# Optimization experiments

Hardware: AMD Instinct MI355X
Metric: run time of the kernel (lower is better)

## Reference

```python
import jax, jax.numpy as jnp
import numpy as np

N = 100000   # nodes
E = 640000   # directed edges
H = 128      # hidden_channels
C = 7        # dataset_num_classes
G = 64       # graphs in the batch
F_IN = 1     # dataset_num_node_features


def setup_inputs() -> dict:
    key = jax.random.key(0)
    ks = jax.random.split(key, 12)
    x = jax.random.normal(ks[0], (N, F_IN), jnp.float32)
    edge_index = jax.random.randint(ks[1], (2, E), 0, N, dtype=jnp.int32)
    batch = jnp.sort(jax.random.randint(ks[2], (N,), 0, G, dtype=jnp.int32))

    def glorot(k, fan_in, fan_out):
        s = jnp.sqrt(6.0 / (fan_in + fan_out)).astype(jnp.float32)
        return jax.random.uniform(k, (fan_in, fan_out), jnp.float32, -s, s)

    return {
        "x": x, "edge_index": edge_index, "batch": batch,
        "W1": glorot(ks[3], F_IN, H), "b1": jnp.zeros((H,), jnp.float32),
        "W2": glorot(ks[4], H, H),    "b2": jnp.zeros((H,), jnp.float32),
        "W3": glorot(ks[5], H, H),    "b3": jnp.zeros((H,), jnp.float32),
        "Wl": glorot(ks[6], H, C),    "bl": jnp.zeros((C,), jnp.float32),
    }


def reference(x, edge_index, batch, W1, b1, W2, b2, W3, b3, Wl, bl):
    n = x.shape[0]
    loop = jnp.arange(n, dtype=edge_index.dtype)
    row = jnp.concatenate([edge_index[0], loop])  # source (message origin)
    col = jnp.concatenate([edge_index[1], loop])  # target (aggregation dst)
    # symmetric normalization D^-1/2 (A+I) D^-1/2 (PyG GCNConv default)
    deg = jax.ops.segment_sum(jnp.ones(row.shape[0], x.dtype), col, num_segments=n)
    dinv = jax.lax.rsqrt(jnp.maximum(deg, 1.0))  # deg >= 1 due to self-loops
    norm = dinv[row] * dinv[col]                 # [E+N]

    def gcn_conv(h, W, b):
        h = h @ W                                # transform first (PyG order)
        msg = h[row] * norm[:, None]             # gather + scale, [E+N, H]
        return jax.ops.segment_sum(msg, col, num_segments=n) + b

    h = jax.nn.relu(gcn_conv(x, W1, b1))
    h = jax.nn.relu(gcn_conv(h, W2, b2))
    h = gcn_conv(h, W3, b3)

    # global mean pool over graph ids; dropout is identity in eval mode
    counts = jax.ops.segment_sum(jnp.ones(n, h.dtype), batch, num_segments=G)
    pooled = jax.ops.segment_sum(h, batch, num_segments=G) / jnp.maximum(counts, 1.0)[:, None]
    return pooled @ Wl + bl
```

## Files before the change

kernel.cpp:

```cpp
#include <hip/hip_runtime.h>

#define HDIM 128
#define NGRAPH 64
#define NCLASS 7
#define PG_NODES 128
#define MAXB 2048

typedef __attribute__((ext_vector_type(8))) __bf16 bf16x8;
typedef __attribute__((ext_vector_type(4))) float f32x4;

__device__ __forceinline__ unsigned short bf16_rne(float f) {
  unsigned u = __float_as_uint(f);
  u += 0x7FFF + ((u >> 16) & 1);
  return (unsigned short)(u >> 16);
}

__device__ __forceinline__ void gload16(const void* g, void* l) {
  __builtin_amdgcn_global_load_lds((const __attribute__((address_space(1))) void*)g,
                                   (__attribute__((address_space(3))) void*)l, 16, 0, 0);
}


__global__ void k_countw(const int* __restrict__ col, const int* __restrict__ row, int E,
                         int* __restrict__ histI, int* __restrict__ histO,
                         const float* __restrict__ W,
                         unsigned short* __restrict__ wthi, unsigned short* __restrict__ wtlo,
                         int cB, int NB) {
  int b = blockIdx.x;
  if (b < cB) {
    __shared__ int binsI[MAXB], binsO[MAXB];
    int t = threadIdx.x;
    for (int i = t; i < NB; i += 256) { binsI[i] = 0; binsO[i] = 0; }
    __syncthreads();
    int base = b << 11;
#pragma unroll
    for (int j = 0; j < 8; j++) {
      int e = base + (j << 8) + t;
      if (e < E) {
        atomicAdd(&binsI[col[e] >> 6], 1);
        atomicAdd(&binsO[row[e] >> 6], 1);
      }
    }
    __syncthreads();
    for (int i = t; i < NB; i += 256) {
      histI[(size_t)b * NB + i] = binsI[i];
      histO[(size_t)b * NB + i] = binsO[i];
    }
  } else {
    int idx = (b - cB) * 256 + threadIdx.x;
    int c = idx >> 7, k = idx & 127;
    float v = W[k * 128 + c];
    unsigned short h = bf16_rne(v);
    wthi[idx] = h;
    wtlo[idx] = bf16_rne(v - __uint_as_float((unsigned)h << 16));
  }
}

__global__ void k_hA(int* __restrict__ histI, int* __restrict__ histO,
                     int* __restrict__ segI, int* __restrict__ segO,
                     int NB, int cB) {
  int bkt = blockIdx.x * 256 + threadIdx.x;
  if (bkt >= NB) return;
  int* hist = blockIdx.z ? histO : histI;
  int* segs = blockIdx.z ? segO : segI;
  int r0 = blockIdx.y << 3;
  int v[8];
#pragma unroll
  for (int j = 0; j < 8; j++) {
    int ri = r0 + j;
    v[j] = (ri < cB) ? hist[(size_t)ri * NB + bkt] : 0;
  }
  int s = 0;
#pragma unroll
  for (int j = 0; j < 8; j++) { int tv = v[j]; v[j] = s; s += tv; }
#pragma unroll
  for (int j = 0; j < 8; j++) {
    int ri = r0 + j;
    if (ri < cB) hist[(size_t)ri * NB + bkt] = v[j];
  }
  segs[(size_t)blockIdx.y * NB + bkt] = s;
}

__global__ void k_hB(int* __restrict__ segI, int* __restrict__ segO,
                     int* __restrict__ btotI, int* __restrict__ btotO,
                     int NB, int NSEG) {
  int bkt = blockIdx.x * 256 + threadIdx.x;
  if (bkt >= NB) return;
  int* segs = blockIdx.y ? segO : segI;
  int* btot = blockIdx.y ? btotO : btotI;
  int run = 0;
  for (int c0 = 0; c0 < NSEG; c0 += 8) {
    int v[8];
#pragma unroll
    for (int j = 0; j < 8; j++) {
      int si = c0 + j;
      v[j] = (si < NSEG) ? segs[(size_t)si * NB + bkt] : 0;
    }
#pragma unroll
    for (int j = 0; j < 8; j++) { int tv = v[j]; v[j] = run; run += tv; }
#pragma unroll
    for (int j = 0; j < 8; j++) {
      int si = c0 + j;
      if (si < NSEG) segs[(size_t)si * NB + bkt] = v[j];
    }
  }
  btot[bkt] = run;
}

__global__ void k_hscanB(const int* __restrict__ btotI, int* __restrict__ boffI,
                         const int* __restrict__ btotO, int* __restrict__ boffO,
                         int NB, int E) {
  __shared__ int sh[1024];
  int t = threadIdx.x;
  for (int s = 0; s < 2; s++) {
    const int* src = s ? btotO : btotI;
    int* boff = s ? boffO : boffI;
    int i0 = 2 * t, i1 = 2 * t + 1;
    int a0 = (i0 < NB) ? src[i0] : 0;
    int a1 = (i1 < NB) ? src[i1] : 0;
    sh[t] = a0 + a1;
    __syncthreads();
    for (int o = 1; o < 1024; o <<= 1) {
      int v = (t >= o) ? sh[t - o] : 0;
      __syncthreads();
      sh[t] += v;
      __syncthreads();
    }
    int ex = (t == 0) ? 0 : sh[t - 1];
    if (i0 < NB) boff[i0] = ex;
    if (i1 < NB) boff[i1] = ex + a0;
    if (t == 0) boff[NB] = E;
    __syncthreads();
  }
}

__global__ void __launch_bounds__(256) k_fill(const int* __restrict__ row,
                                              const int* __restrict__ col, int E,
                                              const int* __restrict__ histI,
                                              const int* __restrict__ histO,
                                              const int* __restrict__ segI,
                                              const int* __restrict__ segO,
                                              const int* __restrict__ boffI,
                                              const int* __restrict__ boffO,
                                              int* __restrict__ inBL,
                                              int* __restrict__ outBL, int NB) {
  __shared__ int baseI[MAXB], baseO[MAXB], binsI[MAXB], binsO[MAXB];
  int t = threadIdx.x, b = blockIdx.x;
  int sg = b >> 3;
  for (int i = t; i < NB; i += 256) {
    baseI[i] = boffI[i] + segI[(size_t)sg * NB + i] + histI[(size_t)b * NB + i];
    baseO[i] = boffO[i] + segO[(size_t)sg * NB + i] + histO[(size_t)b * NB + i];
    binsI[i] = 0;
    binsO[i] = 0;
  }
  __syncthreads();
  int base = b << 11;
#pragma unroll
  for (int j = 0; j < 8; j++) {
    int e = base + (j << 8) + t;
    if (e < E) {
      int r = row[e], c = col[e];
      int rkI = atomicAdd(&binsI[c >> 6], 1);
      int rkO = atomicAdd(&binsO[r >> 6], 1);
      inBL[baseI[c >> 6] + rkI] = (r << 6) | (c & 63);
      outBL[baseO[r >> 6] + rkO] = (c << 6) | (r & 63);
    }
  }
}

__global__ void __launch_bounds__(256) k_rank2x(const int* __restrict__ inBL,
                                                const int* __restrict__ boffI,
                                                const int* __restrict__ batch,
                                                const float* __restrict__ x,
                                                int2* __restrict__ od,
                                                float2* __restrict__ dx,
                                                int* __restrict__ gwi, int n) {
  __shared__ int cnt[64], cnt2[64], loc[64], sc[64];
  int bi = blockIdx.x, t = threadIdx.x;
  if (t < 64) { cnt[t] = 0; cnt2[t] = 0; }
  __syncthreads();
  int e0 = boffI[bi], e1 = boffI[bi + 1];
  for (int e = e0 + t; e < e1; e += 256) atomicAdd(&cnt[inBL[e] & 63], 1);
  __syncthreads();
  if (t < 64) sc[t] = cnt[t];
  __syncthreads();
  for (int o = 1; o < 64; o <<= 1) {
    int v = (t < 64 && t >= o) ? sc[t - o] : 0;
    __syncthreads();
    if (t < 64) sc[t] += v;
    __syncthreads();
  }
  if (t < 64) {
    int excl = (t == 0) ? 0 : sc[t - 1];
    loc[t] = e0 + excl;
    int node = (bi << 6) + t;
    if (node < n) {
      int g = batch[node];
      float dinv = rsqrtf((float)(cnt[t] + 1));
      od[node] = make_int2((e0 + excl) | (g << 24), __float_as_int(dinv));
      dx[node] = make_float2(dinv, x[node]);
    }
  }
  __syncthreads();
  for (int e = e0 + t; e < e1; e += 256) {
    int v = inBL[e];
    int dl = v & 63;
    int k = atomicAdd(&cnt2[dl], 1);
    gwi[loc[dl] + k] = v >> 6;
  }
}

__global__ void k_s(const int2* __restrict__ od, const float2* __restrict__ dx,
                    const int* __restrict__ gwi, float2* __restrict__ sd, int n, int E) {
  int i = blockIdx.x * 256 + threadIdx.x;
  if (i >= n) return;
  int2 o2 = od[i];
  float dinv = __int_as_float(o2.y);
  int e0 = o2.x & 0xFFFFFF;
  int e1 = (i + 1 < n) ? (od[i + 1].x & 0xFFFFFF) : E;
  float s0 = 0.f, s1 = 0.f;
  int e = e0;
  for (; e + 2 <= e1; e += 2) {
    float2 a = dx[gwi[e]];
    float2 b = dx[gwi[e + 1]];
    s0 = fmaf(a.x, a.y, s0);
    s1 = fmaf(b.x, b.y, s1);
  }
  if (e < e1) { float2 a = dx[gwi[e]]; s0 = fmaf(a.x, a.y, s0); }
  float xv = dx[i].y;
  sd[i] = make_float2(fmaf(dinv * dinv, xv, dinv * (s0 + s1)), dinv);
}


__global__ void __launch_bounds__(256) k_l2in(const float2* __restrict__ sd,
                                              const int2* __restrict__ od,
                                              const int* __restrict__ gwi,
                                              const float* __restrict__ W1,
                                              const float* __restrict__ b1,
                                              ushort2* __restrict__ zhi,
                                              ushort2* __restrict__ zlo, int n, int E) {
  int node = blockIdx.x * 4 + (threadIdx.x >> 6);
  if (node >= n) return;
  int l = threadIdx.x & 63;
  float2 w1 = ((const float2*)W1)[l];
  float2 bv = ((const float2*)b1)[l];
  int2 on = od[node];
  float dstd = __int_as_float(on.y);
  float nself = dstd * dstd;
  float sv = sd[node].x;
  float2 acc;
  acc.x = nself * fmaxf(fmaf(sv, w1.x, bv.x), 0.f);
  acc.y = nself * fmaxf(fmaf(sv, w1.y, bv.y), 0.f);
  int e0 = on.x & 0xFFFFFF;
  int e1 = (node + 1 < n) ? (od[node + 1].x & 0xFFFFFF) : E;

  for (int eb = e0; eb < e1; eb += 64) {
    int m = e1 - eb; if (m > 64) m = 64;
    int ee = eb + l; if (ee >= e1) ee = e1 - 1;
    float2 q = sd[gwi[ee]];
    float u = q.y * dstd;
    int k = 0;
    for (; k + 4 <= m; k += 4) {
      float q0 = __shfl(q.x, k),     u0 = __shfl(u, k);
      float q1 = __shfl(q.x, k + 1), u1 = __shfl(u, k + 1);
      float q2 = __shfl(q.x, k + 2), u2 = __shfl(u, k + 2);
      float q3 = __shfl(q.x, k + 3), u3 = __shfl(u, k + 3);
      acc.x = fmaf(u0, fmaxf(fmaf(q0, w1.x, bv.x), 0.f), acc.x);
      acc.y = fmaf(u0, fmaxf(fmaf(q0, w1.y, bv.y), 0.f), acc.y);
      acc.x = fmaf(u1, fmaxf(fmaf(q1, w1.x, bv.x), 0.f), acc.x);
      acc.y = fmaf(u1, fmaxf(fmaf(q1, w1.y, bv.y), 0.f), acc.y);
      acc.x = fmaf(u2, fmaxf(fmaf(q2, w1.x, bv.x), 0.f), acc.x);
      acc.y = fmaf(u2, fmaxf(fmaf(q2, w1.y, bv.y), 0.f), acc.y);
      acc.x = fmaf(u3, fmaxf(fmaf(q3, w1.x, bv.x), 0.f), acc.x);
      acc.y = fmaf(u3, fmaxf(fmaf(q3, w1.y, bv.y), 0.f), acc.y);
    }
    for (; k < m; k++) {
      float qk = __shfl(q.x, k), uk = __shfl(u, k);
      acc.x = fmaf(uk, fmaxf(fmaf(qk, w1.x, bv.x), 0.f), acc.x);
      acc.y = fmaf(uk, fmaxf(fmaf(qk, w1.y, bv.y), 0.f), acc.y);
    }
  }

  ushort2 h, lo;
  h.x = bf16_rne(acc.x);
  lo.x = bf16_rne(acc.x - __uint_as_float((unsigned)h.x << 16));
  h.y = bf16_rne(acc.y);
  lo.y = bf16_rne(acc.y - __uint_as_float((unsigned)h.y << 16));
  zhi[(size_t)node * 64 + l] = h;
  zlo[(size_t)node * 64 + l] = lo;
}


__global__ void __launch_bounds__(256)
k_gemm_mfma(const unsigned short* __restrict__ zhi, const unsigned short* __restrict__ zlo,
            const unsigned short* __restrict__ whi, const unsigned short* __restrict__ wlo,
            const float* __restrict__ bias, float* __restrict__ out, int n) {
  __shared__ uint4 lds[2048];
  const int t = threadIdx.x;
  const int l = t & 63, wv = t >> 6;
  const int wr = wv >> 1, wc = wv & 1;
  const int lr = l & 15, lk = l >> 4;
  const int rowBase = blockIdx.x << 7;
  const bool full = (rowBase + 128 <= n);

  f32x4 acc[4][4];
#pragma unroll
  for (int mt = 0; mt < 4; mt++)
#pragma unroll
    for (int nt = 0; nt < 4; nt++) acc[mt][nt] = (f32x4){0.f, 0.f, 0.f, 0.f};

  for (int ch = 0; ch < 4; ch++) {
    __syncthreads();
    if (full) {
#pragma unroll
      for (int i = 0; i < 2; i++) {
        int s = t + (i << 8);
        int sl = s & 63, rt = s >> 6;
        int row = rowBase + (rt << 4) + (sl & 15);
        int kk = (ch << 5) + ((sl >> 4) << 3);
        gload16(&zhi[(size_t)row * 128 + kk], &lds[s]);
        gload16(&zlo[(size_t)row * 128 + kk], &lds[512 + s]);
      }
    } else {
#pragma unroll
      for (int i = 0; i < 2; i++) {
        int s = t + (i << 8);
        int sl = s & 63, rt = s >> 6;
        int row = rowBase + (rt << 4) + (sl & 15);
        int kk = (ch << 5) + ((sl >> 4) << 3);
        uint4 vh = make_uint4(0u, 0u, 0u, 0u), vl = vh;
        if (row < n) {
          vh = *(const uint4*)&zhi[(size_t)row * 128 + kk];
          vl = *(const uint4*)&zlo[(size_t)row * 128 + kk];
        }
        lds[s] = vh;
        lds[512 + s] = vl;
      }
    }
#pragma unroll
    for (int i = 0; i < 2; i++) {
      int s = t + (i << 8);
      int sl = s & 63, ct = s >> 6;
      int col = (ct << 4) + (sl & 15);
      int kk = (ch << 5) + ((sl >> 4) << 3);
      gload16(&whi[col * 128 + kk], &lds[1024 + s]);
      gload16(&wlo[col * 128 + kk], &lds[1536 + s]);
    }
    __syncthreads();

    bf16x8 ah[4], al[4], bh[4], bl[4];
#pragma unroll
    for (int mt = 0; mt < 4; mt++) {
      int slot = ((wr << 2) + mt) * 64 + l;
      ah[mt] = *(const bf16x8*)&lds[slot];
      al[mt] = *(const bf16x8*)&lds[512 + slot];
    }
#pragma unroll
    for (int nt = 0; nt < 4; nt++) {
      int slot = ((wc << 2) + nt) * 64 + l;
      bh[nt] = *(const bf16x8*)&lds[1024 + slot];
      bl[nt] = *(const bf16x8*)&lds[1536 + slot];
    }
#pragma unroll
    for (int mt = 0; mt < 4; mt++)
#pragma unroll
      for (int nt = 0; nt < 4; nt++) {
        acc[mt][nt] = __builtin_amdgcn_mfma_f32_16x16x32_bf16(ah[mt], bh[nt], acc[mt][nt], 0, 0, 0);
        acc[mt][nt] = __builtin_amdgcn_mfma_f32_16x16x32_bf16(ah[mt], bl[nt], acc[mt][nt], 0, 0, 0);
        acc[mt][nt] = __builtin_amdgcn_mfma_f32_16x16x32_bf16(al[mt], bh[nt], acc[mt][nt], 0, 0, 0);
      }
  }

  float bv[4];
#pragma unroll
  for (int nt = 0; nt < 4; nt++) bv[nt] = bias[(wc << 6) + (nt << 4) + lr];
#pragma unroll
  for (int mt = 0; mt < 4; mt++) {
    int rbase = rowBase + (wr << 6) + (mt << 4) + (lk << 2);
#pragma unroll
    for (int j = 0; j < 4; j++) {
      int row = rbase + j;
      if (row < n) {
#pragma unroll
        for (int nt = 0; nt < 4; nt++) {
          int c2 = (wc << 6) + (nt << 4) + lr;
          out[(size_t)row * 128 + c2] = fmaxf(acc[mt][nt][j] + bv[nt], 0.f);
        }
      }
    }
  }
}


__global__ void __launch_bounds__(256) k_pgemm(const float* __restrict__ H,
                                               const int* __restrict__ outBL,
                                               const int* __restrict__ boff,
                                               const int2* __restrict__ od,
                                               float* __restrict__ partials, int n) {
  __shared__ float4 Hl4[64 * 32];
  __shared__ float4 Pl4[64 * 16];
  __shared__ float dinvL[64];
  float* Pl = (float*)Pl4;
  const int t = threadIdx.x;
  const int jl = t & 31;
  const int gq = (t >> 5) << 1;
  float4 acc[8];
#pragma unroll
  for (int i = 0; i < 8; i++) acc[i] = make_float4(0.f, 0.f, 0.f, 0.f);
  const int base0 = blockIdx.x * PG_NODES;

  for (int sub = 0; sub < PG_NODES / 64; sub++) {
    const int base = base0 + sub * 64;
    __syncthreads();
    if (base + 64 <= n) {
      for (int l = t; l < 2048; l += 256)
        gload16(&H[(size_t)(base + (l >> 5)) * 128 + ((l & 31) << 2)], &Hl4[l]);
    } else {
      for (int l = t; l < 2048; l += 256) {
        int i = l >> 5, q = l & 31;
        int node = base + i;
        Hl4[l] = (node < n) ? *(const float4*)&H[(size_t)node * 128 + (q << 2)]
                            : make_float4(0.f, 0.f, 0.f, 0.f);
      }
    }
    for (int l = t; l < 1024; l += 256) Pl4[l] = make_float4(0.f, 0.f, 0.f, 0.f);
    __syncthreads();
    if (t < 64) {
      int node = base + t;
      float dv = 0.f;
      if (node < n) {
        int2 o2 = od[node];
        dv = __int_as_float(o2.y);
        atomicAdd(&Pl[(t << 6) + (int)(((unsigned)o2.x) >> 24)], dv * dv);
      }
      dinvL[t] = dv;
    }
    __syncthreads();
    int e0 = 0, e1 = 0;
    if (base < n) {
      int bi = base >> 6;
      e0 = boff[bi];
      e1 = boff[bi + 1];
    }
    for (int e = e0 + t; e < e1; e += 256) {
      int p = outBL[e];
      int2 oc = od[p >> 6];
      float w2 = dinvL[p & 63] * __int_as_float(oc.y);
      atomicAdd(&Pl[((p & 63) << 6) + (int)(((unsigned)oc.x) >> 24)], w2);
    }
    __syncthreads();

#define FMA4(A, PV) \
  A.x = fmaf(PV, hv.x, A.x); A.y = fmaf(PV, hv.y, A.y); \
  A.z = fmaf(PV, hv.z, A.z); A.w = fmaf(PV, hv.w, A.w);
#pragma unroll 4
    for (int i = 0; i < 64; i++) {
      float4 hv = Hl4[i * 32 + jl];
      float4 pa = Pl4[i * 16 + gq];
      float4 pb = Pl4[i * 16 + gq + 1];
      FMA4(acc[0], pa.x) FMA4(acc[1], pa.y) FMA4(acc[2], pa.z) FMA4(acc[3], pa.w)
      FMA4(acc[4], pb.x) FMA4(acc[5], pb.y) FMA4(acc[6], pb.z) FMA4(acc[7], pb.w)
    }
#undef FMA4
  }

  float* dst = &partials[(size_t)blockIdx.x * (NGRAPH * HDIM)];
  int gb = (t >> 5) << 3;
#pragma unroll
  for (int gi = 0; gi < 8; gi++)
    *(float4*)&dst[(gb + gi) * HDIM + (jl << 2)] = acc[gi];
}

__global__ void k_reduce(const float* __restrict__ partials, float* __restrict__ pooled,
                         int nparts) {
  int cell = blockIdx.x * 256 + threadIdx.x;
  int stride = gridDim.y;
  int p = blockIdx.y;
  float a0 = 0.f, a1 = 0.f, a2 = 0.f, a3 = 0.f;
  for (; p + 3 * stride < nparts; p += 4 * stride) {
    a0 += partials[(size_t)p * 8192 + cell];
    a1 += partials[(size_t)(p + stride) * 8192 + cell];
    a2 += partials[(size_t)(p + 2 * stride) * 8192 + cell];
    a3 += partials[(size_t)(p + 3 * stride) * 8192 + cell];
  }
  for (; p < nparts; p += stride) a0 += partials[(size_t)p * 8192 + cell];
  unsafeAtomicAdd(&pooled[cell], (a0 + a1) + (a2 + a3));
}

__global__ void k_mid(const float* __restrict__ pooled, const int* __restrict__ batch, int n,
                      const float* __restrict__ W3, const float* __restrict__ b3,
                      const float* __restrict__ Wl, const float* __restrict__ bl,
                      float* __restrict__ out) {
  __shared__ float sh[HDIM];
  __shared__ float invSh;
  int g = blockIdx.x, j = threadIdx.x;
  if (j == 0) {
    int lo = 0, hi = n;
    while (lo < hi) { int m = (lo + hi) >> 1; if (batch[m] < g) lo = m + 1; else hi = m; }
    int a = lo;
    lo = 0; hi = n;
    while (lo < hi) { int m = (lo + hi) >> 1; if (batch[m] < g + 1) lo = m + 1; else hi = m; }
    invSh = 1.f / fmaxf((float)(lo - a), 1.f);
  }
  __syncthreads();
  float inv = invSh;
  float acc = 0.f;
  for (int k = 0; k < HDIM; k++) acc = fmaf(pooled[g * HDIM + k], W3[k * HDIM + j], acc);
  sh[j] = acc * inv + b3[j];
  __syncthreads();
  if (j < NCLASS) {
    float o = bl[j];
    for (int k = 0; k < HDIM; k++) o = fmaf(sh[k], Wl[k * NCLASS + j], o);
    out[g * NCLASS + j] = o;
  }
}


extern "C" void kernel_launch(void* const* d_in, const int* in_sizes, int n_in,
                              void* d_out, int out_size, void* d_ws, size_t ws_size,
                              hipStream_t stream) {
  const float* x   = (const float*)d_in[0];
  const int*   ei  = (const int*)d_in[1];
  const int*   bat = (const int*)d_in[2];
  const float* W1  = (const float*)d_in[3];
  const float* b1  = (const float*)d_in[4];
  const float* W2  = (const float*)d_in[5];
  const float* b2  = (const float*)d_in[6];
  const float* W3  = (const float*)d_in[7];
  const float* b3  = (const float*)d_in[8];
  const float* Wl  = (const float*)d_in[9];
  const float* bl  = (const float*)d_in[10];
  float* out = (float*)d_out;

  const int n = in_sizes[0];
  const int E = in_sizes[1] / 2;
  const int* rowv = ei;
  const int* colv = ei + E;
  const int NB = (n + 63) >> 6;
  const int cB = (E + 2047) / 2048;
  const int NSEG = (cB + 7) >> 3;

  char* w = (char*)d_ws;
  size_t o = 0;
  auto alloc = [&](size_t bytes) {
    size_t r = (o + 255) & ~(size_t)255;
    o = r + bytes;
    return r;
  };
  const int nPB = (n + PG_NODES - 1) / PG_NODES;

  size_t o_pool  = alloc((size_t)NGRAPH * HDIM * 4);
  size_t zero_end = o;
  size_t o_histI = alloc((size_t)cB * NB * 4);
  size_t o_histO = alloc((size_t)cB * NB * 4);
  size_t o_segI  = alloc((size_t)NSEG * NB * 4);
  size_t o_segO  = alloc((size_t)NSEG * NB * 4);
  size_t o_btotI = alloc((size_t)MAXB * 4);
  size_t o_btotO = alloc((size_t)MAXB * 4);
  size_t o_boffI = alloc((size_t)(MAXB + 1) * 4);
  size_t o_boffO = alloc((size_t)(MAXB + 1) * 4);
  size_t o_od    = alloc((size_t)n * 8);
  size_t o_dx    = alloc((size_t)n * 8);
  size_t o_sd    = alloc((size_t)n * 8);
  size_t o_wt    = alloc((size_t)HDIM * HDIM * 4);
  size_t o_gw    = alloc((size_t)E * 4);
  size_t o_inBL  = alloc((size_t)E * 4);
  size_t o_outBL = alloc((size_t)E * 4);
  size_t o_bufA  = alloc((size_t)n * HDIM * 4);
  size_t o_bufB  = alloc((size_t)n * HDIM * 4);
  (void)n_in; (void)out_size; (void)ws_size;

  float*  pooled   = (float*)(w + o_pool);
  int*    histI    = (int*)(w + o_histI);
  int*    histO    = (int*)(w + o_histO);
  int*    segI     = (int*)(w + o_segI);
  int*    segO     = (int*)(w + o_segO);
  int*    btotI    = (int*)(w + o_btotI);
  int*    btotO    = (int*)(w + o_btotO);
  int*    boffI    = (int*)(w + o_boffI);
  int*    boffO    = (int*)(w + o_boffO);
  int2*   od       = (int2*)(w + o_od);
  float2* dx       = (float2*)(w + o_dx);
  float2* sd       = (float2*)(w + o_sd);
  unsigned short* wthi = (unsigned short*)(w + o_wt);
  unsigned short* wtlo = wthi + HDIM * HDIM;
  int*    gwi      = (int*)(w + o_gw);
  int*    inBL     = (int*)(w + o_inBL);
  int*    outBL    = (int*)(w + o_outBL);
  float*  bufA     = (float*)(w + o_bufA);
  unsigned short* zhi = (unsigned short*)(w + o_bufB);
  unsigned short* zlo = zhi + (size_t)n * HDIM;
  float*  partials = (float*)(w + o_bufB);

  hipMemsetAsync(w + o_pool, 0, zero_end - o_pool, stream);

  const int gB = (NB + 255) / 256;
  k_countw<<<cB + 64, 256, 0, stream>>>(colv, rowv, E, histI, histO, W2,
                                        wthi, wtlo, cB, NB);
  k_hA<<<dim3(gB, NSEG, 2), 256, 0, stream>>>(histI, histO, segI, segO, NB, cB);
  k_hB<<<dim3(gB, 2), 256, 0, stream>>>(segI, segO, btotI, btotO, NB, NSEG);
  k_hscanB<<<1, 1024, 0, stream>>>(btotI, boffI, btotO, boffO, NB, E);
  k_fill<<<cB, 256, 0, stream>>>(rowv, colv, E, histI, histO, segI, segO,
                                 boffI, boffO, inBL, outBL, NB);
  k_rank2x<<<NB, 256, 0, stream>>>(inBL, boffI, bat, x, od, dx, gwi, n);
  k_s<<<(n + 255) / 256, 256, 0, stream>>>(od, dx, gwi, sd, n, E);

  k_l2in<<<(n + 3) / 4, 256, 0, stream>>>(sd, od, gwi, W1, b1,
                                          (ushort2*)zhi, (ushort2*)zlo, n, E);

  k_gemm_mfma<<<(n + 127) / 128, 256, 0, stream>>>(zhi, zlo, wthi, wtlo, b2, bufA, n);

  k_pgemm<<<nPB, 256, 0, stream>>>(bufA, outBL, boffO, od, partials, n);
  k_reduce<<<dim3(32, 8), 256, 0, stream>>>(partials, pooled, nPB);

  k_mid<<<NGRAPH, HDIM, 0, stream>>>(pooled, bat, n, W3, b3, Wl, bl, out);
}
```

Before: 250.0 us.

## Fuse MFMA layer-2 GEMM with pooled-propagation GEMM via shared LDS union

Merges the bf16-split MFMA GEMM kernel and the per-block pooling GEMM into one kernel. The relu'd GEMM tile stays in registers and is written to an LDS union instead of round-tripping a full N x 128 fp32 buffer through global memory. This removes one kernel launch and about 100 MB of global write and read traffic. In exchange, LDS use per block grows to about 48 KB, which may lower occupancy, and partials now get their own workspace allocation.

Result: faster. 242.8 us (-2.8%).

```diff
diff --git a/kernel.cpp b/kernel.cpp
--- a/kernel.cpp
+++ b/kernel.cpp
@@ -3,7 +3,6 @@
 #define HDIM 128
 #define NGRAPH 64
 #define NCLASS 7
-#define PG_NODES 128
 #define MAXB 2048
 
 typedef __attribute__((ext_vector_type(8))) __bf16 bf16x8;
@@ -291,11 +290,19 @@
 }
 
 
+union SmemU {
+  uint4 stage[2048];
+  struct { float Hf[64 * 128]; float Pl[64 * 64]; } pg;
+};
+
 __global__ void __launch_bounds__(256)
-k_gemm_mfma(const unsigned short* __restrict__ zhi, const unsigned short* __restrict__ zlo,
-            const unsigned short* __restrict__ whi, const unsigned short* __restrict__ wlo,
-            const float* __restrict__ bias, float* __restrict__ out, int n) {
-  __shared__ uint4 lds[2048];
+k_gemm_pg(const unsigned short* __restrict__ zhi, const unsigned short* __restrict__ zlo,
+          const unsigned short* __restrict__ whi, const unsigned short* __restrict__ wlo,
+          const float* __restrict__ bias, const int* __restrict__ outBL,
+          const int* __restrict__ boffO, const int2* __restrict__ od,
+          float* __restrict__ partials, int n) {
+  __shared__ SmemU u;
+  __shared__ float dinvL[64];
   const int t = threadIdx.x;
   const int l = t & 63, wv = t >> 6;
   const int wr = wv >> 1, wc = wv & 1;
@@ -318,8 +325,8 @@
         int sl = s & 63, rt = s >> 6;
         int row = rowBase + (rt << 4) + (sl & 15);
         int kk = (ch << 5) + ((sl >> 4) << 3);
-        gload16(&zhi[(size_t)row * 128 + kk], &lds[s]);
-        gload16(&zlo[(size_t)row * 128 + kk], &lds[512 + s]);
+        gload16(&zhi[(size_t)row * 128 + kk], &u.stage[s]);
+        gload16(&zlo[(size_t)row * 128 + kk], &u.stage[512 + s]);
       }
     } else {
 #pragma unroll
@@ -333,8 +340,8 @@
           vh = *(const uint4*)&zhi[(size_t)row * 128 + kk];
           vl = *(const uint4*)&zlo[(size_t)row * 128 + kk];
         }
-        lds[s] = vh;
-        lds[512 + s] = vl;
+        u.stage[s] = vh;
+        u.stage[512 + s] = vl;
       }
     }
 #pragma unroll
@@ -343,8 +350,8 @@
       int sl = s & 63, ct = s >> 6;
       int col = (ct << 4) + (sl & 15);
       int kk = (ch << 5) + ((sl >> 4) << 3);
-      gload16(&whi[col * 128 + kk], &lds[1024 + s]);
-      gload16(&wlo[col * 128 + kk], &lds[1536 + s]);
+      gload16(&whi[col * 128 + kk], &u.stage[1024 + s]);
+      gload16(&wlo[col * 128 + kk], &u.stage[1536 + s]);
     }
     __syncthreads();
 
@@ -352,14 +359,14 @@
 #pragma unroll
     for (int mt = 0; mt < 4; mt++) {
       int slot = ((wr << 2) + mt) * 64 + l;
-      ah[mt] = *(const bf16x8*)&lds[slot];
-      al[mt] = *(const bf16x8*)&lds[512 + slot];
+      ah[mt] = *(const bf16x8*)&u.stage[slot];
+      al[mt] = *(const bf16x8*)&u.stage[512 + slot];
     }
 #pragma unroll
     for (int nt = 0; nt < 4; nt++) {
       int slot = ((wc << 2) + nt) * 64 + l;
-      bh[nt] = *(const bf16x8*)&lds[1024 + slot];
-      bl[nt] = *(const bf16x8*)&lds[1536 + slot];
+      bh[nt] = *(const bf16x8*)&u.stage[1024 + slot];
+      bl[nt] = *(const bf16x8*)&u.stage[1536 + slot];
     }
 #pragma unroll
     for (int mt = 0; mt < 4; mt++)
@@ -375,55 +382,35 @@
 #pragma unroll
   for (int nt = 0; nt < 4; nt++) bv[nt] = bias[(wc << 6) + (nt << 4) + lr];
 #pragma unroll
-  for (int mt = 0; mt < 4; mt++) {
-    int rbase = rowBase + (wr << 6) + (mt << 4) + (lk << 2);
-#pragma unroll
-    for (int j = 0; j < 4; j++) {
-      int row = rbase + j;
-      if (row < n) {
-#pragma unroll
-        for (int nt = 0; nt < 4; nt++) {
-          int c2 = (wc << 6) + (nt << 4) + lr;
-          out[(size_t)row * 128 + c2] = fmaxf(acc[mt][nt][j] + bv[nt], 0.f);
-        }
-      }
-    }
-  }
-}
-
-
-__global__ void __launch_bounds__(256) k_pgemm(const float* __restrict__ H,
-                                               const int* __restrict__ outBL,
-                                               const int* __restrict__ boff,
-                                               const int2* __restrict__ od,
-                                               float* __restrict__ partials, int n) {
-  __shared__ float4 Hl4[64 * 32];
-  __shared__ float4 Pl4[64 * 16];
-  __shared__ float dinvL[64];
-  float* Pl = (float*)Pl4;
-  const int t = threadIdx.x;
+  for (int mt = 0; mt < 4; mt++)
+#pragma unroll
+    for (int nt = 0; nt < 4; nt++)
+#pragma unroll
+      for (int j = 0; j < 4; j++)
+        acc[mt][nt][j] = fmaxf(acc[mt][nt][j] + bv[nt], 0.f);
+
   const int jl = t & 31;
   const int gq = (t >> 5) << 1;
-  float4 acc[8];
-#pragma unroll
-  for (int i = 0; i < 8; i++) acc[i] = make_float4(0.f, 0.f, 0.f, 0.f);
-  const int base0 = blockIdx.x * PG_NODES;
-
-  for (int sub = 0; sub < PG_NODES / 64; sub++) {
-    const int base = base0 + sub * 64;
-    __syncthreads();
-    if (base + 64 <= n) {
-      for (int l = t; l < 2048; l += 256)
-        gload16(&H[(size_t)(base + (l >> 5)) * 128 + ((l & 31) << 2)], &Hl4[l]);
-    } else {
-      for (int l = t; l < 2048; l += 256) {
-        int i = l >> 5, q = l & 31;
-        int node = base + i;
-        Hl4[l] = (node < n) ? *(const float4*)&H[(size_t)node * 128 + (q << 2)]
-                            : make_float4(0.f, 0.f, 0.f, 0.f);
-      }
-    }
-    for (int l = t; l < 1024; l += 256) Pl4[l] = make_float4(0.f, 0.f, 0.f, 0.f);
+  float4 acc2[8];
+#pragma unroll
+  for (int i = 0; i < 8; i++) acc2[i] = make_float4(0.f, 0.f, 0.f, 0.f);
+
+  for (int sub = 0; sub < 2; sub++) {
+    const int base = rowBase + (sub << 6);
+    __syncthreads();
+    for (int i4 = t; i4 < 1024; i4 += 256) ((float4*)u.pg.Pl)[i4] = make_float4(0.f, 0.f, 0.f, 0.f);
+    if (wr == sub) {
+#pragma unroll
+      for (int mt = 0; mt < 4; mt++)
+#pragma unroll
+        for (int j = 0; j < 4; j++) {
+          int li = (mt << 4) + (lk << 2) + j;
+          bool ok = (base + li) < n;
+#pragma unroll
+          for (int nt = 0; nt < 4; nt++)
+            u.pg.Hf[li * 128 + (wc << 6) + (nt << 4) + lr] = ok ? acc[mt][nt][j] : 0.f;
+        }
+    }
     __syncthreads();
     if (t < 64) {
       int node = base + t;
@@ -431,7 +418,7 @@
       if (node < n) {
         int2 o2 = od[node];
         dv = __int_as_float(o2.y);
-        atomicAdd(&Pl[(t << 6) + (int)(((unsigned)o2.x) >> 24)], dv * dv);
+        atomicAdd(&u.pg.Pl[(t << 6) + (int)(((unsigned)o2.x) >> 24)], dv * dv);
       }
       dinvL[t] = dv;
     }
@@ -439,14 +426,14 @@
     int e0 = 0, e1 = 0;
     if (base < n) {
       int bi = base >> 6;
-      e0 = boff[bi];
-      e1 = boff[bi + 1];
+      e0 = boffO[bi];
+      e1 = boffO[bi + 1];
     }
     for (int e = e0 + t; e < e1; e += 256) {
       int p = outBL[e];
       int2 oc = od[p >> 6];
       float w2 = dinvL[p & 63] * __int_as_float(oc.y);
-      atomicAdd(&Pl[((p & 63) << 6) + (int)(((unsigned)oc.x) >> 24)], w2);
+      atomicAdd(&u.pg.Pl[((p & 63) << 6) + (int)(((unsigned)oc.x) >> 24)], w2);
     }
     __syncthreads();
 
@@ -455,11 +442,11 @@
   A.z = fmaf(PV, hv.z, A.z); A.w = fmaf(PV, hv.w, A.w);
 #pragma unroll 4
     for (int i = 0; i < 64; i++) {
-      float4 hv = Hl4[i * 32 + jl];
-      float4 pa = Pl4[i * 16 + gq];
-      float4 pb = Pl4[i * 16 + gq + 1];
-      FMA4(acc[0], pa.x) FMA4(acc[1], pa.y) FMA4(acc[2], pa.z) FMA4(acc[3], pa.w)
-      FMA4(acc[4], pb.x) FMA4(acc[5], pb.y) FMA4(acc[6], pb.z) FMA4(acc[7], pb.w)
+      float4 hv = *(const float4*)&u.pg.Hf[i * 128 + (jl << 2)];
+      float4 pa = ((const float4*)u.pg.Pl)[i * 16 + gq];
+      float4 pb = ((const float4*)u.pg.Pl)[i * 16 + gq + 1];
+      FMA4(acc2[0], pa.x) FMA4(acc2[1], pa.y) FMA4(acc2[2], pa.z) FMA4(acc2[3], pa.w)
+      FMA4(acc2[4], pb.x) FMA4(acc2[5], pb.y) FMA4(acc2[6], pb.z) FMA4(acc2[7], pb.w)
     }
 #undef FMA4
   }
@@ -468,7 +455,7 @@
   int gb = (t >> 5) << 3;
 #pragma unroll
   for (int gi = 0; gi < 8; gi++)
-    *(float4*)&dst[(gb + gi) * HDIM + (jl << 2)] = acc[gi];
+    *(float4*)&dst[(gb + gi) * HDIM + (jl << 2)] = acc2[gi];
 }
 
 __global__ void k_reduce(const float* __restrict__ partials, float* __restrict__ pooled,
@@ -539,6 +526,7 @@
   const int NB = (n + 63) >> 6;
   const int cB = (E + 2047) / 2048;
   const int NSEG = (cB + 7) >> 3;
+  const int nPB = (n + 127) >> 7;
 
   char* w = (char*)d_ws;
   size_t o = 0;
@@ -547,7 +535,6 @@
     o = r + bytes;
     return r;
   };
-  const int nPB = (n + PG_NODES - 1) / PG_NODES;
 
   size_t o_pool  = alloc((size_t)NGRAPH * HDIM * 4);
   size_t zero_end = o;
@@ -566,7 +553,7 @@
   size_t o_gw    = alloc((size_t)E * 4);
   size_t o_inBL  = alloc((size_t)E * 4);
   size_t o_outBL = alloc((size_t)E * 4);
-  size_t o_bufA  = alloc((size_t)n * HDIM * 4);
+  size_t o_part  = alloc((size_t)nPB * NGRAPH * HDIM * 4);
   size_t o_bufB  = alloc((size_t)n * HDIM * 4);
   (void)n_in; (void)out_size; (void)ws_size;
 
@@ -587,10 +574,9 @@
   int*    gwi      = (int*)(w + o_gw);
   int*    inBL     = (int*)(w + o_inBL);
   int*    outBL    = (int*)(w + o_outBL);
-  float*  bufA     = (float*)(w + o_bufA);
+  float*  partials = (float*)(w + o_part);
   unsigned short* zhi = (unsigned short*)(w + o_bufB);
   unsigned short* zlo = zhi + (size_t)n * HDIM;
-  float*  partials = (float*)(w + o_bufB);
 
   hipMemsetAsync(w + o_pool, 0, zero_end - o_pool, stream);
 
@@ -608,9 +594,8 @@
   k_l2in<<<(n + 3) / 4, 256, 0, stream>>>(sd, od, gwi, W1, b1,
                                           (ushort2*)zhi, (ushort2*)zlo, n, E);
 
-  k_gemm_mfma<<<(n + 127) / 128, 256, 0, stream>>>(zhi, zlo, wthi, wtlo, b2, bufA, n);
-
-  k_pgemm<<<nPB, 256, 0, stream>>>(bufA, outBL, boffO, od, partials, n);
+  k_gemm_pg<<<nPB, 256, 0, stream>>>(zhi, zlo, wthi, wtlo, b2, outBL, boffO, od,
+                                     partials, n);
   k_reduce<<<dim3(32, 8), 256, 0, stream>>>(partials, pooled, nPB);
 
   k_mid<<<NGRAPH, HDIM, 0, stream>>>(pooled, bat, n, W3, b3, Wl, bl, out);
```
